# Optimization experiments

Hardware: AMD Instinct MI355X
Metric: run time of the kernel (lower is better)

## Reference

```python
import jax, jax.numpy as jnp
import numpy as np

B, N, D, E = 2, 50000, 64, 800000


def setup_inputs() -> dict:
    key = jax.random.key(0)
    k = jax.random.split(key, 6)
    return {
        "prev_embeddings": jax.random.normal(k[0], (B, N, D), dtype=jnp.float32),
        "edges_ij": jax.random.randint(k[1], (E, 2), 0, N, dtype=jnp.int64 if jax.config.jax_enable_x64 else jnp.int32),
        "node_features_embeddings": jax.random.normal(k[2], (B, N, D), dtype=jnp.float32),
        "edge_features_embeddings": jax.random.normal(k[3], (B, N, D), dtype=jnp.float32),
        "edge_status": jax.random.uniform(k[4], (E,), dtype=jnp.float32),
        "W": jax.random.normal(k[5], (D, D), dtype=jnp.float32) / np.sqrt(D).astype(np.float32),
    }


def reference(prev_embeddings, edges_ij, node_features_embeddings, edge_features_embeddings, edge_status, W):
    # prev_embeddings: (B, N, D); edges_ij: (E, 2); edge_status: (E,) in [0,1]; W: (D, D) theta2 weight (no bias)
    u = edges_ij[:, 0]
    v = edges_ij[:, 1]
    g = edge_status.astype(prev_embeddings.dtype).reshape(1, -1, 1)  # broadcast (1,E,1) over batch
    h_u = prev_embeddings[:, u, :] * g  # gather source endpoint, gate
    h_v = prev_embeddings[:, v, :] * g  # gather dest endpoint, gate
    # scatter-add gated messages in both directions: nbr[b, v] += h_u, nbr[b, u] += h_v
    nbr = jnp.zeros_like(prev_embeddings).at[:, v, :].add(h_u).at[:, u, :].add(h_v)
    x2 = jnp.einsum('bnd,ed->bne', nbr, W)  # Linear(D,D,bias=False): nbr @ W.T
    return jax.nn.leaky_relu(node_features_embeddings + x2 + edge_features_embeddings)
```

## Files before the change

kernel.cpp:

```cpp
#include <hip/hip_runtime.h>

constexpr int B = 2;
constexpr int N = 50000;
constexpr int D = 64;
constexpr int E = 800000;
constexpr int CAP = 96;
constexpr int XG = 8;
constexpr int NPG = N / XG;
constexpr int ECHUNKS = E / 256;
constexpr int PBLOCKS = (B * N) / 4;

__device__ __forceinline__ unsigned f2bf(float f) {
    unsigned u = __float_as_uint(f);
    return (u + 0x7FFFu + ((u >> 16) & 1u)) >> 16;
}
__device__ __forceinline__ float bfhi2f(unsigned bits) {
    return __uint_as_float(bits & 0xFFFF0000u);
}
__device__ __forceinline__ float bflo2f(unsigned bits) {
    return __uint_as_float(bits << 16);
}

__global__ __launch_bounds__(256) void build_pgemm_fused(
    const int2* __restrict__ edges, const float* __restrict__ status,
    int* __restrict__ counts, unsigned* __restrict__ slots,
    const float* __restrict__ prev, const float* __restrict__ W,
    unsigned* __restrict__ P32)
{
    __shared__ float Wl[D][D + 1];

    int grp = blockIdx.x >> 3;
    int sub8 = blockIdx.x & 7;
    int t = threadIdx.x;

    if ((grp & 1) == 0) {
        int e = (grp >> 1) * 256 + t;
        int2 uv = edges[e];
        unsigned gb = f2bf(status[e]) << 16;
        if (uv.x / NPG == sub8) {
            int p = atomicAdd(&counts[uv.x], 1);
            if (p < CAP) slots[(size_t)uv.x * CAP + p] = gb | (unsigned)uv.y;
        }
        if (uv.y / NPG == sub8) {
            int p = atomicAdd(&counts[uv.y], 1);
            if (p < CAP) slots[(size_t)uv.y * CAP + p] = gb | (unsigned)uv.x;
        }
    } else {
        int pb = (grp >> 1) * 8 + sub8;
        for (int i = t; i < D * D; i += 256) Wl[i >> 6][i & 63] = W[i];
        __syncthreads();

        int wave = t >> 6, lane = t & 63;
        int row = __builtin_amdgcn_readfirstlane(pb * 4 + wave);
        const float* pr = prev + (size_t)row * D;

        float acc = 0.f;
#pragma unroll
        for (int d = 0; d < D; ++d) acc += pr[d] * Wl[lane][d];

        float partner = __shfl_xor(acc, 1, 64);
        if ((lane & 1) == 0) {
            P32[(size_t)row * 32 + (lane >> 1)] = f2bf(acc) | (f2bf(partner) << 16);
        }
    }
}

__global__ __launch_bounds__(256) void gather_final(
    const uint4* __restrict__ P4,
    const int* __restrict__ counts,
    const unsigned* __restrict__ slots,
    const float* __restrict__ node,
    const float* __restrict__ edgef,
    float* __restrict__ out)
{
    __shared__ float xs[4][2][D];

    int t = threadIdx.x;
    int wave = t >> 6, lane = t & 63;
    int n = blockIdx.x * 4 + wave;
    int j = lane & 7;
    int sub = lane >> 3;

    int cnt = min(counts[n], CAP);
    size_t sbase = (size_t)n * CAP;

    float a0[8], a1[8];
#pragma unroll
    for (int i = 0; i < 8; ++i) { a0[i] = 0.f; a1[i] = 0.f; }

    for (int k = sub; k < cnt; k += 8) {
        unsigned ent = slots[sbase + k];
        float g = bfhi2f(ent);
        unsigned nb = ent & 0xFFFFu;
        uint4 r0 = P4[(size_t)nb * 8 + j];
        uint4 r1 = P4[((size_t)N + nb) * 8 + j];
        a0[0] += g * bflo2f(r0.x); a0[1] += g * bfhi2f(r0.x);
        a0[2] += g * bflo2f(r0.y); a0[3] += g * bfhi2f(r0.y);
        a0[4] += g * bflo2f(r0.z); a0[5] += g * bfhi2f(r0.z);
        a0[6] += g * bflo2f(r0.w); a0[7] += g * bfhi2f(r0.w);
        a1[0] += g * bflo2f(r1.x); a1[1] += g * bfhi2f(r1.x);
        a1[2] += g * bflo2f(r1.y); a1[3] += g * bfhi2f(r1.y);
        a1[4] += g * bflo2f(r1.z); a1[5] += g * bfhi2f(r1.z);
        a1[6] += g * bflo2f(r1.w); a1[7] += g * bfhi2f(r1.w);
    }

#pragma unroll
    for (int m = 8; m <= 32; m <<= 1) {
#pragma unroll
        for (int i = 0; i < 8; ++i) {
            a0[i] += __shfl_xor(a0[i], m, 64);
            a1[i] += __shfl_xor(a1[i], m, 64);
        }
    }

    if (sub == 0) {
        *(float4*)&xs[wave][0][j * 8]     = make_float4(a0[0], a0[1], a0[2], a0[3]);
        *(float4*)&xs[wave][0][j * 8 + 4] = make_float4(a0[4], a0[5], a0[6], a0[7]);
        *(float4*)&xs[wave][1][j * 8]     = make_float4(a1[0], a1[1], a1[2], a1[3]);
        *(float4*)&xs[wave][1][j * 8 + 4] = make_float4(a1[4], a1[5], a1[6], a1[7]);
    }
    float s0 = xs[wave][0][lane];
    float s1 = xs[wave][1][lane];

    size_t b0 = (size_t)n * D + lane;
    size_t b1 = (size_t)N * D + b0;
    float y0 = node[b0] + s0 + edgef[b0];
    float y1 = node[b1] + s1 + edgef[b1];
    out[b0] = (y0 >= 0.f) ? y0 : 0.01f * y0;
    out[b1] = (y1 >= 0.f) ? y1 : 0.01f * y1;
}

__device__ inline void atomic_add4(float* p, float4 val, float g) {
    atomicAdd(p + 0, val.x * g);
    atomicAdd(p + 1, val.y * g);
    atomicAdd(p + 2, val.z * g);
    atomicAdd(p + 3, val.w * g);
}

__global__ __launch_bounds__(256) void scatter_kernel(
    const float* __restrict__ prev,
    const int2* __restrict__ edges,
    const float* __restrict__ status,
    float* __restrict__ nbr)
{
    int idx = blockIdx.x * 256 + threadIdx.x;
    int e = idx >> 4;
    int q = idx & 15;
    if (e >= E) return;
    int2 uv = edges[e];
    float g = status[e];
    const float4* p0 = (const float4*)prev;
    const float4* p1 = (const float4*)(prev + (size_t)N * D);
    float4 pu0 = p0[(size_t)uv.x * 16 + q];
    float4 pv0 = p0[(size_t)uv.y * 16 + q];
    float4 pu1 = p1[(size_t)uv.x * 16 + q];
    float4 pv1 = p1[(size_t)uv.y * 16 + q];
    float* n0 = nbr;
    float* n1 = nbr + (size_t)N * D;
    int off_v = uv.y * D + q * 4;
    int off_u = uv.x * D + q * 4;
    atomic_add4(n0 + off_v, pu0, g);
    atomic_add4(n0 + off_u, pv0, g);
    atomic_add4(n1 + off_v, pu1, g);
    atomic_add4(n1 + off_u, pv1, g);
}

__global__ __launch_bounds__(256) void gemm_relu_kernel(
    float* __restrict__ out,
    const float* __restrict__ node,
    const float* __restrict__ edgef,
    const float* __restrict__ W)
{
    __shared__ float Wl[D][D + 1];
    __shared__ float xs[4][D];
    int t = threadIdx.x;
    for (int i = t; i < D * D; i += 256) Wl[i >> 6][i & 63] = W[i];
    int wave = t >> 6, lane = t & 63;
    int row = blockIdx.x * 4 + wave;
    size_t base = (size_t)row * D;
    float x = out[base + lane];
    xs[wave][lane] = x;
    __syncthreads();
    float acc = 0.f;
#pragma unroll
    for (int d = 0; d < D; ++d) acc += xs[wave][d] * Wl[lane][d];
    float y = node[base + lane] + acc + edgef[base + lane];
    out[base + lane] = (y >= 0.f) ? y : 0.01f * y;
}

extern "C" void kernel_launch(void* const* d_in, const int* in_sizes, int n_in,
                              void* d_out, int out_size, void* d_ws, size_t ws_size,
                              hipStream_t stream) {
    const float* prev   = (const float*)d_in[0];
    const int*   edges  = (const int*)d_in[1];
    const float* node   = (const float*)d_in[2];
    const float* edgef  = (const float*)d_in[3];
    const float* status = (const float*)d_in[4];
    const float* W      = (const float*)d_in[5];
    float* out = (float*)d_out;

    const int2* edges2 = (const int2*)edges;

    size_t slots_bytes  = (size_t)N * CAP * sizeof(unsigned);
    size_t counts_bytes = (size_t)N * sizeof(int);
    size_t p_bytes      = (size_t)B * N * 32 * sizeof(unsigned);
    size_t need = slots_bytes + counts_bytes + p_bytes;

    if (ws_size >= need) {
        unsigned* slots = (unsigned*)d_ws;
        int* counts = (int*)((char*)d_ws + slots_bytes);
        unsigned* P32 = (unsigned*)((char*)d_ws + slots_bytes + counts_bytes);

        hipMemsetAsync(counts, 0, counts_bytes, stream);
        build_pgemm_fused<<<ECHUNKS * XG + PBLOCKS, 256, 0, stream>>>(
            edges2, status, counts, slots, prev, W, P32);
        gather_final<<<N / 4, 256, 0, stream>>>(
            (const uint4*)P32, counts, slots, node, edgef, out);
    } else {
        hipMemsetAsync(out, 0, (size_t)B * N * D * sizeof(float), stream);
        scatter_kernel<<<(E * 16) / 256, 256, 0, stream>>>(prev, edges2, status, out);
        gemm_relu_kernel<<<(B * N) / 4, 256, 0, stream>>>(out, node, edgef, W);
    }
}
```

Measured before the change: 303.0 us.

## Persistent P-GEMM waves with W held in registers, interleaved 25:1 with edge chunks

Replaces one-row-per-wave P blocks, each of which reloaded W into LDS, with far fewer blocks that each process 25 rows per wave while keeping the W row in registers. The edge-bucketing and GEMM work are now interleaved at a 25:1 group ratio instead of 1:1. This removes the repeated W staging, the block barriers and most of the block launch overhead. In exchange it raises register pressure and gives coarser work granularity for the GEMM part.

```diff
diff --git a/kernel.cpp b/kernel.cpp
--- a/kernel.cpp
+++ b/kernel.cpp
@@ -8,7 +8,10 @@
 constexpr int XG = 8;
 constexpr int NPG = N / XG;
 constexpr int ECHUNKS = E / 256;
-constexpr int PBLOCKS = (B * N) / 4;
+
+constexpr int ROWS_PER_WAVE = 25;
+constexpr int PGROUPS = 125;
+constexpr int TOTAL_GROUPS = ECHUNKS + PGROUPS;
 
 __device__ __forceinline__ unsigned f2bf(float f) {
     unsigned u = __float_as_uint(f);
@@ -27,14 +30,16 @@
     const float* __restrict__ prev, const float* __restrict__ W,
     unsigned* __restrict__ P32)
 {
-    __shared__ float Wl[D][D + 1];
-
     int grp = blockIdx.x >> 3;
     int sub8 = blockIdx.x & 7;
     int t = threadIdx.x;
 
-    if ((grp & 1) == 0) {
-        int e = (grp >> 1) * 256 + t;
+    int nm = grp / 26;
+    int pos = grp % 26;
+
+    if (pos < 25) {
+        int chunk = nm * 25 + pos;
+        int e = chunk * 256 + t;
         int2 uv = edges[e];
         unsigned gb = f2bf(status[e]) << 16;
         if (uv.x / NPG == sub8) {
@@ -46,21 +51,32 @@
             if (p < CAP) slots[(size_t)uv.y * CAP + p] = gb | (unsigned)uv.x;
         }
     } else {
-        int pb = (grp >> 1) * 8 + sub8;
-        for (int i = t; i < D * D; i += 256) Wl[i >> 6][i & 63] = W[i];
-        __syncthreads();
-
+        int pb = nm * 8 + sub8;
         int wave = t >> 6, lane = t & 63;
-        int row = __builtin_amdgcn_readfirstlane(pb * 4 + wave);
-        const float* pr = prev + (size_t)row * D;
-
-        float acc = 0.f;
-#pragma unroll
-        for (int d = 0; d < D; ++d) acc += pr[d] * Wl[lane][d];
-
-        float partner = __shfl_xor(acc, 1, 64);
-        if ((lane & 1) == 0) {
-            P32[(size_t)row * 32 + (lane >> 1)] = f2bf(acc) | (f2bf(partner) << 16);
+
+        const float4* W4 = (const float4*)W;
+        float4 w[16];
+#pragma unroll
+        for (int q = 0; q < 16; ++q) w[q] = W4[lane * 16 + q];
+
+        int row0 = pb * (4 * ROWS_PER_WAVE) + wave * ROWS_PER_WAVE;
+        for (int r = 0; r < ROWS_PER_WAVE; ++r) {
+            int row = __builtin_amdgcn_readfirstlane(row0 + r);
+            const float* pr = prev + (size_t)row * D;
+
+            float acc = 0.f;
+#pragma unroll
+            for (int d = 0; d < D; ++d) {
+                const float4& wq = w[d >> 2];
+                float wd = (d & 3) == 0 ? wq.x : (d & 3) == 1 ? wq.y
+                         : (d & 3) == 2 ? wq.z : wq.w;
+                acc += pr[d] * wd;
+            }
+
+            float partner = __shfl_xor(acc, 1, 64);
+            if ((lane & 1) == 0) {
+                P32[(size_t)row * 32 + (lane >> 1)] = f2bf(acc) | (f2bf(partner) << 16);
+            }
         }
     }
 }
@@ -212,7 +228,7 @@
         unsigned* P32 = (unsigned*)((char*)d_ws + slots_bytes + counts_bytes);
 
         hipMemsetAsync(counts, 0, counts_bytes, stream);
-        build_pgemm_fused<<<ECHUNKS * XG + PBLOCKS, 256, 0, stream>>>(
+        build_pgemm_fused<<<TOTAL_GROUPS * 8, 256, 0, stream>>>(
             edges2, status, counts, slots, prev, W, P32);
         gather_final<<<N / 4, 256, 0, stream>>>(
             (const uint4*)P32, counts, slots, node, edgef, out);
```

Result: slower. 312.8 us (+3.2%).
